# Performance work log

Hardware: AMD Instinct MI355X
Metric: run time of the kernel (lower is better)

Reference implementation:

```python
import jax, jax.numpy as jnp
import numpy as np

BS, SL, D = 4, 2048, 1024
H = 16
HD = D // H  # 64


def setup_inputs() -> dict:
    key = jax.random.key(0)
    ks = jax.random.split(key, 11)
    s = 1.0 / np.sqrt(D)
    inp = {
        "value": jax.random.normal(ks[0], (BS, SL, D), jnp.float32),
        "key_in": jax.random.normal(ks[1], (BS, SL, D), jnp.float32),
        "query": jax.random.normal(ks[2], (BS, SL, D), jnp.float32),
        # nn.Linear weights stored [out, in] (torch convention); orthogonal-ish init approximated by scaled normal
        "Wq": jax.random.normal(ks[3], (D, D), jnp.float32) * s,
        "bq": jax.random.normal(ks[4], (D,), jnp.float32) * 0.01,
        "Wk": jax.random.normal(ks[5], (D, D), jnp.float32) * s,
        "bk": jax.random.normal(ks[6], (D,), jnp.float32) * 0.01,
        "Wv": jax.random.normal(ks[7], (D, D), jnp.float32) * s,
        "bv": jax.random.normal(ks[8], (D,), jnp.float32) * 0.01,
        "Wo": jax.random.normal(ks[9], (D, D), jnp.float32) * s,
        "bo": jax.random.normal(ks[10], (D,), jnp.float32) * 0.01,
    }
    return inp


def reference(value, key_in, query, Wq, bq, Wk, bk, Wv, bv, Wo, bo):
    bs, sl, _ = value.shape
    # projections (torch Linear: x @ W.T + b), then split heads -> [b, h, s, hd]
    def proj(x, W, b):
        return (x @ W.T + b).reshape(bs, -1, H, HD).transpose(0, 2, 1, 3)

    q = proj(query, Wq, bq)
    k = proj(key_in, Wk, bk)
    v = proj(value, Wv, bv)

    scale = 1.0 / jnp.sqrt(jnp.asarray(HD, q.dtype))
    logits = jnp.einsum("bhqd,bhkd->bhqk", q, k) * scale  # [b,h,s,s]
    # amax-subtract + softmax == stable softmax
    attn = jax.nn.softmax(logits, axis=-1)
    out = jnp.einsum("bhqk,bhkd->bhqd", attn, v)
    out = out.transpose(0, 2, 1, 3).reshape(bs, sl, D)  # [b,s,D]
    o = out @ Wo.T + bo
    return o
```

## Files before the change

kernel.cpp:

```cpp
#include <hip/hip_runtime.h>
#include <hip/hip_bf16.h>

typedef __bf16 bf16_t;
typedef __bf16 bf16x8 __attribute__((ext_vector_type(8)));
typedef __bf16 bf16x4 __attribute__((ext_vector_type(4)));
typedef float f32x4 __attribute__((ext_vector_type(4)));
typedef float f32x16 __attribute__((ext_vector_type(16)));

#define BS 4
#define SL 2048
#define DM 1024
#define NH 16
#define HD 64

static __device__ __forceinline__ bf16_t tobf(float x) { return (bf16_t)x; }

#if __has_builtin(__builtin_amdgcn_exp2f)
#define EXP2(x) __builtin_amdgcn_exp2f(x)
#else
#define EXP2(x) exp2f(x)
#endif

#if __has_builtin(__builtin_amdgcn_cvt_pk_bf16_f32)
typedef __bf16 bf16x2_t __attribute__((ext_vector_type(2)));
static __device__ __forceinline__ uint32_t pack_bf16(float a, float b) {
  union { bf16x2_t v; uint32_t u; } c;
  c.v = __builtin_amdgcn_cvt_pk_bf16_f32(a, b);
  return c.u;
}
#else
static __device__ __forceinline__ uint32_t pack_bf16(float a, float b) {
  union { bf16_t e[2]; uint32_t u; } c;
  c.e[0] = tobf(a); c.e[1] = tobf(b);
  return c.u;
}
#endif

static __device__ __forceinline__ void glds16(const void* g, void* l) {
  __builtin_amdgcn_global_load_lds(
      (const __attribute__((address_space(1))) void*)g,
      (__attribute__((address_space(3))) void*)l, 16, 0, 0);
}

#define BAR()    asm volatile("s_barrier" ::: "memory")
#define WAITV0() asm volatile("s_waitcnt vmcnt(0)" ::: "memory")
#define WAITV4() asm volatile("s_waitcnt vmcnt(4)" ::: "memory")
#define WAITLG() asm volatile("s_waitcnt lgkmcnt(0)" ::: "memory")
#define SCHEDB() __builtin_amdgcn_sched_barrier(0)

__global__ void convert_w_kernel(const float* __restrict__ s0, const float* __restrict__ s1,
                                 const float* __restrict__ s2, const float* __restrict__ s3,
                                 bf16_t* __restrict__ d0, bf16_t* __restrict__ d1,
                                 bf16_t* __restrict__ d2, bf16_t* __restrict__ d3)
{
  const float* s; bf16_t* d;
  switch (blockIdx.y) {
    case 0: s = s0; d = d0; break;
    case 1: s = s1; d = d1; break;
    case 2: s = s2; d = d2; break;
    default: s = s3; d = d3; break;
  }
  int i = (blockIdx.x * 256 + threadIdx.x) * 4;
  float4 v = *(const float4*)(s + i);
  bf16x4 o; o[0] = tobf(v.x); o[1] = tobf(v.y); o[2] = tobf(v.z); o[3] = tobf(v.w);
  *(bf16x4*)(d + i) = o;
}

__global__ void convert_a_kernel(const float* __restrict__ q, const float* __restrict__ k,
                                 const float* __restrict__ v, bf16_t* __restrict__ dst)
{
  const float* s = blockIdx.y == 0 ? q : (blockIdx.y == 1 ? k : v);
  bf16_t* d = dst + (size_t)blockIdx.y * ((size_t)BS * SL * DM);
  int i = (blockIdx.x * 256 + threadIdx.x) * 4;
  float4 x = *(const float4*)(s + i);
  bf16x4 o; o[0] = tobf(x.x); o[1] = tobf(x.y); o[2] = tobf(x.z); o[3] = tobf(x.w);
  *(bf16x4*)(d + i) = o;
}

__global__ __launch_bounds__(512, 2) void gemm_qkv_kernel(
    const bf16_t* __restrict__ Aall, const bf16_t* __restrict__ Wcat,
    const float* __restrict__ bq, const float* __restrict__ bk, const float* __restrict__ bvv,
    bf16_t* __restrict__ Qb, bf16_t* __restrict__ Kbo, bf16_t* __restrict__ Vtb)
{
  __shared__ __align__(16) char sMem[131072];

  const int tid  = threadIdx.x;
  const int wave = tid >> 6;
  const int lane = tid & 63;
  const int l15  = lane & 15;
  const int quad = lane >> 4;
  const int wr   = wave >> 2;
  const int wc   = wave & 3;
  const int m0 = blockIdx.x * 256;
  const int nTile = blockIdx.y;
  const int proj = nTile >> 2;
  const int n0 = (nTile & 3) * 256;
  const int nW = nTile * 256;

  const bf16_t* Af = Aall + (size_t)proj * ((size_t)BS * SL * DM);
  const float* bias = proj == 0 ? bq : (proj == 1 ? bk : bvv);

  auto stageA = [&](int u) {
    int tu = u >> 1, kk = u & 1;
    char* dst = sMem + (u & 3) * 16384;
#pragma unroll
    for (int g2 = 0; g2 < 2; g2++) {
      int slot = wave * 2 + g2;
      int f = slot * 64 + lane;
      int row = f >> 2;
      int cg = (f & 3) ^ (row & 3);
      glds16(Af + (size_t)(m0 + row) * DM + tu * 64 + kk * 32 + cg * 8,
             dst + slot * 1024);
    }
  };
  auto stageB = [&](int u) {
    int tu = u >> 1, kk = u & 1;
    char* dst = sMem + 65536 + (u & 3) * 16384;
#pragma unroll
    for (int g2 = 0; g2 < 2; g2++) {
      int slot = wave * 2 + g2;
      int f = slot * 64 + lane;
      int row = f >> 2;
      int cg = (f & 3) ^ (row & 3);
      glds16(Wcat + (size_t)(nW + row) * DM + tu * 64 + kk * 32 + cg * 8,
             dst + slot * 1024);
    }
  };

  f32x4 acc[8][4];
#pragma unroll
  for (int i = 0; i < 8; i++)
#pragma unroll
    for (int j = 0; j < 4; j++) acc[i][j] = f32x4{0.f, 0.f, 0.f, 0.f};

  stageA(0); stageB(0); stageA(1); stageB(1); stageA(2); stageB(2);
  WAITV4(); SCHEDB();
  BAR();

  bf16x8 b[4];
  for (int T = 0; T < 16; ++T) {
#pragma unroll
    for (int p = 0; p < 4; ++p) {
      const int qm = p & 1, kk = p >> 1;
      const int ubuf = (2 * T + kk) & 3;
      const char* ab = sMem + ubuf * 16384;
      const char* bb = sMem + 65536 + ubuf * 16384;

      bf16x8 a[4];
#pragma unroll
      for (int mf = 0; mf < 4; mf++) {
        int row = wr * 128 + qm * 64 + mf * 16 + l15;
        a[mf] = *(const bf16x8*)(ab + row * 64 + ((quad ^ (row & 3)) * 16));
      }
      if (qm == 0) {
#pragma unroll
        for (int nf = 0; nf < 4; nf++) {
          int row = wc * 64 + nf * 16 + l15;
          b[nf] = *(const bf16x8*)(bb + row * 64 + ((quad ^ (row & 3)) * 16));
        }
      }

      if (p == 0)      { int u = 2 * T + 3; if (u < 32) stageA(u); }
      else if (p == 1) { int u = 2 * T + 3; if (u < 32) stageB(u); }
      else if (p == 2) { int u = 2 * T + 4; if (u < 32) stageA(u); }
      else             { int u = 2 * T + 4; if (u < 32) stageB(u); }

      if (p == 3 && T < 15) {
        if (T == 14) { WAITV0(); } else { WAITV4(); }
        SCHEDB();
      }
      BAR();
      WAITLG(); SCHEDB();
      __builtin_amdgcn_s_setprio(1);
#pragma unroll
      for (int mf = 0; mf < 4; mf++)
#pragma unroll
        for (int nf = 0; nf < 4; nf++)
          acc[qm * 4 + mf][nf] = __builtin_amdgcn_mfma_f32_16x16x32_bf16(
              a[mf], b[nf], acc[qm * 4 + mf][nf], 0, 0, 0);
      __builtin_amdgcn_s_setprio(0);
      BAR();
    }
  }

  if (proj < 2) {
    bf16_t* C = proj == 0 ? Qb : Kbo;
#pragma unroll
    for (int nf = 0; nf < 4; nf++) {
      int col = n0 + wc * 64 + nf * 16 + l15;
      float bv = bias[col];
#pragma unroll
      for (int i = 0; i < 8; i++) {
        int rowb = m0 + wr * 128 + (i >> 2) * 64 + (i & 3) * 16 + quad * 4;
#pragma unroll
        for (int r = 0; r < 4; r++)
          C[(size_t)(rowb + r) * DM + col] = tobf(acc[i][nf][r] + bv);
      }
    }
  } else {
#pragma unroll
    for (int nf = 0; nf < 4; nf++) {
      int col = n0 + wc * 64 + nf * 16 + l15;
      float bv = bias[col];
      int head = col >> 6, hd = col & 63;
#pragma unroll
      for (int i = 0; i < 8; i++) {
        int rowb = m0 + wr * 128 + (i >> 2) * 64 + (i & 3) * 16 + quad * 4;
        int bidx = rowb >> 11, s = rowb & (SL - 1);
        bf16x4 o;
#pragma unroll
        for (int r = 0; r < 4; r++) o[r] = tobf(acc[i][nf][r] + bv);
        *(bf16x4*)(Vtb + ((size_t)(bidx * NH + head) * HD + hd) * SL + s) = o;
      }
    }
  }
}

__global__ __launch_bounds__(256, 2) void gemm_out_kernel(
    const bf16_t* __restrict__ A, const bf16_t* __restrict__ Bw,
    const float* __restrict__ bias, float* __restrict__ C)
{
  __shared__ __align__(16) char sMem[32768];

  const int tid  = threadIdx.x;
  const int wave = tid >> 6;
  const int lane = tid & 63;
  const int l15  = lane & 15;
  const int quad = lane >> 4;
  const int m0 = blockIdx.x * 128;
  const int n0 = blockIdx.y * 128;
  const int wm = (wave & 1) * 64;
  const int wn = (wave >> 1) * 64;

  auto stage = [&](int r, int k0) {
    char* base = sMem + r * 16384;
#pragma unroll
    for (int t = 0; t < 2; t++) {
      int slot = wave * 2 + t;
      int f = slot * 64 + lane;
      int row = f >> 2;
      int cg = (f & 3) ^ (row & 3);
      glds16(A  + (size_t)(m0 + row) * DM + k0 + cg * 8, base + slot * 1024);
      glds16(Bw + (size_t)(n0 + row) * DM + k0 + cg * 8, base + 8192 + slot * 1024);
    }
  };

  f32x4 acc[4][4];
#pragma unroll
  for (int i = 0; i < 4; i++)
#pragma unroll
    for (int j = 0; j < 4; j++) acc[i][j] = f32x4{0.f, 0.f, 0.f, 0.f};

  stage(0, 0);
  for (int t = 0; t < 32; ++t) {
    __syncthreads();
    if (t < 31) stage((t + 1) & 1, (t + 1) * 32);

    const bf16_t* sA = (const bf16_t*)(sMem + (t & 1) * 16384);
    const bf16_t* sB = sA + 4096;

    bf16x8 af[4], bfr[4];
#pragma unroll
    for (int i = 0; i < 4; i++) {
      int row = wm + i * 16 + l15;
      af[i] = *(const bf16x8*)(sA + row * 32 + (quad ^ (row & 3)) * 8);
    }
#pragma unroll
    for (int j = 0; j < 4; j++) {
      int row = wn + j * 16 + l15;
      bfr[j] = *(const bf16x8*)(sB + row * 32 + (quad ^ (row & 3)) * 8);
    }

#pragma unroll
    for (int i = 0; i < 4; i++)
#pragma unroll
      for (int j = 0; j < 4; j++)
        acc[i][j] = __builtin_amdgcn_mfma_f32_16x16x32_bf16(af[i], bfr[j], acc[i][j], 0, 0, 0);
  }

#pragma unroll
  for (int j = 0; j < 4; j++) {
    int col = n0 + wn + j * 16 + l15;
    float bv = bias[col];
#pragma unroll
    for (int i = 0; i < 4; i++) {
      int rowb = m0 + wm + i * 16 + quad * 4;
#pragma unroll
      for (int r = 0; r < 4; r++)
        C[(size_t)(rowb + r) * DM + col] = acc[i][j][r] + bv;
    }
  }
}

__global__ __launch_bounds__(256, 4) void attn_kernel(
    const bf16_t* __restrict__ Q, const bf16_t* __restrict__ Kb,
    const bf16_t* __restrict__ Vt, bf16_t* __restrict__ O)
{
  __shared__ __align__(16) char sMem[32768];

  const int tid  = threadIdx.x;
  const int wave = tid >> 6;
  const int lane = tid & 63;
  const int l31  = lane & 31;
  const int h    = lane >> 5;
  const int swl  = l31 & 7;

  const int id  = blockIdx.x;
  const int xcd = id & 7, slot = id >> 3;
  const int bh  = xcd * 8 + (slot >> 4);
  const int qi  = slot & 15;
  const int b = bh >> 4, hh = bh & 15;
  const int q0 = qi * 128 + wave * 32;

  auto stage = [&](int r, int k0) {
    char* base = sMem + r * 16384;
#pragma unroll
    for (int t = 0; t < 2; t++) {
      int slot2 = wave * 2 + t;
      int f = slot2 * 64 + lane;
      int row = f >> 3;
      int cg = (f & 7) ^ ((row + (row >> 3)) & 7);
      glds16(Kb + (size_t)(b * SL + k0 + row) * DM + hh * HD + cg * 8,
             base + slot2 * 1024);
      glds16(Vt + ((size_t)bh * HD + row) * SL + k0 + cg * 8,
             base + 8192 + slot2 * 1024);
    }
  };

  bf16x8 qf[4];
  {
    const bf16_t* qp = Q + (size_t)(b * SL + q0 + l31) * DM + hh * HD + h * 8;
#pragma unroll
    for (int c = 0; c < 4; c++) {
      bf16x8 v = *(const bf16x8*)(qp + c * 16);
#pragma unroll
      for (int j = 0; j < 8; j++) v[j] = tobf((float)v[j] * 0.18033688f);
      qf[c] = v;
    }
  }

  f32x16 o_acc[2];
#pragma unroll
  for (int m = 0; m < 2; m++)
#pragma unroll
    for (int r = 0; r < 16; r++) o_acc[m][r] = 0.f;
  float rs0 = 0.f, rs1 = 0.f;

  stage(0, 0);
  for (int t = 0; t < 32; ++t) {
    __syncthreads();
    if (t < 31) stage((t + 1) & 1, (t + 1) * 64);

    const bf16_t* sK = (const bf16_t*)(sMem + (t & 1) * 16384);
    const bf16_t* sV = sK + 4096;

#pragma unroll
    for (int s = 0; s < 2; s++) {
      int rowK = s * 32 + l31;
      int kkK = (rowK + (rowK >> 3)) & 7;
      bf16x8 kf[4];
#pragma unroll
      for (int c = 0; c < 4; c++)
        kf[c] = *(const bf16x8*)(sK + rowK * 64 + (((c * 2 + h) ^ kkK) * 8));

      f32x16 st;
#pragma unroll
      for (int r = 0; r < 16; r++) st[r] = -17.312340f;
#pragma unroll
      for (int c = 0; c < 4; c++)
        st = __builtin_amdgcn_mfma_f32_32x32x16_bf16(kf[c], qf[c], st, 0, 0, 0);

      uint32_t w[8];
#pragma unroll
      for (int i = 0; i < 8; i++) {
        float p0 = EXP2(st[2 * i]);
        float p1 = EXP2(st[2 * i + 1]);
        rs0 += p0; rs1 += p1;
        w[i] = pack_bf16(p0, p1);
      }
      uint32_t y0 = (uint32_t)__shfl_xor((int)(h ? w[0] : w[2]), 32);
      uint32_t y1 = (uint32_t)__shfl_xor((int)(h ? w[1] : w[3]), 32);
      uint32_t y2 = (uint32_t)__shfl_xor((int)(h ? w[4] : w[6]), 32);
      uint32_t y3 = (uint32_t)__shfl_xor((int)(h ? w[5] : w[7]), 32);
      union { uint32_t u[4]; bf16x8 v; } pf0, pf1;
      pf0.u[0] = h ? y0   : w[0];
      pf0.u[1] = h ? y1   : w[1];
      pf0.u[2] = h ? w[2] : y0;
      pf0.u[3] = h ? w[3] : y1;
      pf1.u[0] = h ? y2   : w[4];
      pf1.u[1] = h ? y3   : w[5];
      pf1.u[2] = h ? w[6] : y2;
      pf1.u[3] = h ? w[7] : y3;

#pragma unroll
      for (int m = 0; m < 2; m++) {
        int rowV = m * 32 + l31;
        int kkV = (rowV + (rowV >> 3)) & 7;
#pragma unroll
        for (int c = 0; c < 2; c++) {
          int chunk = (s * 4 + c * 2 + h) ^ kkV;
          bf16x8 vf = *(const bf16x8*)(sV + rowV * 64 + chunk * 8);
          o_acc[m] = __builtin_amdgcn_mfma_f32_32x32x16_bf16(
              vf, (c ? pf1.v : pf0.v), o_acc[m], 0, 0, 0);
        }
      }
    }
  }

  float rs = rs0 + rs1;
  rs += __shfl_xor(rs, 32);
  float inv = 1.f / rs;
  bf16_t* so = (bf16_t*)sMem + wave * 2048;
#pragma unroll
  for (int m = 0; m < 2; m++) {
#pragma unroll
    for (int r = 0; r < 16; r++) {
      int hd = m * 32 + (r & 3) + 8 * (r >> 2) + 4 * h;
      so[l31 * 64 + (((hd >> 3) ^ swl) * 8) + (hd & 7)] = tobf(o_acc[m][r] * inv);
    }
  }
  asm volatile("s_waitcnt lgkmcnt(0)" ::: "memory");
  {
    int qr = lane >> 1, hf = lane & 1;
    int sw2 = qr & 7;
#pragma unroll
    for (int cc = 0; cc < 4; cc++) {
      int chunk = (hf * 4 + cc) ^ sw2;
      bf16x8 v = *(const bf16x8*)(so + qr * 64 + chunk * 8);
      *(bf16x8*)(O + (size_t)(b * SL + q0 + qr) * DM + hh * HD + hf * 32 + cc * 8) = v;
    }
  }
}

extern "C" void kernel_launch(void* const* d_in, const int* in_sizes, int n_in,
                              void* d_out, int out_size, void* d_ws, size_t ws_size,
                              hipStream_t stream)
{
  const float* value  = (const float*)d_in[0];
  const float* key_in = (const float*)d_in[1];
  const float* query  = (const float*)d_in[2];
  const float* Wq = (const float*)d_in[3];
  const float* bq = (const float*)d_in[4];
  const float* Wk = (const float*)d_in[5];
  const float* bk = (const float*)d_in[6];
  const float* Wv = (const float*)d_in[7];
  const float* bv = (const float*)d_in[8];
  const float* Wo = (const float*)d_in[9];
  const float* bo = (const float*)d_in[10];

  char* ws = (char*)d_ws;
  const size_t sz  = (size_t)BS * SL * DM * sizeof(bf16_t);
  const size_t wsz = (size_t)DM * DM * sizeof(bf16_t);
  bf16_t* Qb   = (bf16_t*)(ws + 0 * sz);
  bf16_t* Kb   = (bf16_t*)(ws + 1 * sz);
  bf16_t* Ob   = (bf16_t*)(ws + 2 * sz);
  bf16_t* Vtb  = (bf16_t*)(ws + 3 * sz);
  bf16_t* Wcat = (bf16_t*)(ws + 4 * sz);
  bf16_t* Wob  = (bf16_t*)(ws + 4 * sz + 3 * wsz);
  bf16_t* Abf  = (bf16_t*)(ws + 4 * sz + 4 * wsz);

  const int M = BS * SL;

  convert_w_kernel<<<dim3(1024, 4), 256, 0, stream>>>(
      Wq, Wk, Wv, Wo, Wcat, Wcat + DM * DM, Wcat + 2 * DM * DM, Wob);

  convert_a_kernel<<<dim3(M * DM / 1024, 3), 256, 0, stream>>>(
      query, key_in, value, Abf);

  gemm_qkv_kernel<<<dim3(M / 256, 12), 512, 0, stream>>>(
      Abf, Wcat, bq, bk, bv, Qb, Kb, Vtb);

  attn_kernel<<<dim3(SL / 128 * BS * NH), 256, 0, stream>>>(Qb, Kb, Vtb, Ob);

  gemm_out_kernel<<<dim3(M / 128, DM / 128), 256, 0, stream>>>(Ob, Wob, bo, (float*)d_out);
}
```

Measured before the change: 359.3 us.

## Retile QKV and output GEMMs, swap lane shuffles for permlane32 swap

The QKV GEMM drops from a 256x256 to a 128x256 tile, with a 4-stage 32-wide K pipeline and a unified A+B staging lambda. This shrinks shared memory and doubles the grid for better CU occupancy. The output GEMM moves from a double-buffered 128x128 tile on 256 threads to the same 512-thread 128x256 pipelined scheme. In attention, the cross-half lane exchange uses v_permlane32_swap instead of ds_bpermute shuffles, and the MFMA blocks get s_setprio boosts. The risk is lower per-block reuse in the QKV GEMM and reliance on the permlane32 swap semantics matching the old select-and-shuffle logic.

```diff
diff --git a/kernel.cpp b/kernel.cpp
--- a/kernel.cpp
+++ b/kernel.cpp
@@ -36,6 +36,10 @@
 }
 #endif
 
+static __device__ __forceinline__ void permswap(uint32_t& a, uint32_t& b) {
+  asm("v_permlane32_swap_b32 %0, %1" : "+v"(a), "+v"(b));
+}
+
 static __device__ __forceinline__ void glds16(const void* g, void* l) {
   __builtin_amdgcn_global_load_lds(
       (const __attribute__((address_space(1))) void*)g,
@@ -44,7 +48,8 @@
 
 #define BAR()    asm volatile("s_barrier" ::: "memory")
 #define WAITV0() asm volatile("s_waitcnt vmcnt(0)" ::: "memory")
-#define WAITV4() asm volatile("s_waitcnt vmcnt(4)" ::: "memory")
+#define WAITV3() asm volatile("s_waitcnt vmcnt(3)" ::: "memory")
+#define WAITV6() asm volatile("s_waitcnt vmcnt(6)" ::: "memory")
 #define WAITLG() asm volatile("s_waitcnt lgkmcnt(0)" ::: "memory")
 #define SCHEDB() __builtin_amdgcn_sched_barrier(0)
 
@@ -82,7 +87,7 @@
     const float* __restrict__ bq, const float* __restrict__ bk, const float* __restrict__ bvv,
     bf16_t* __restrict__ Qb, bf16_t* __restrict__ Kbo, bf16_t* __restrict__ Vtb)
 {
-  __shared__ __align__(16) char sMem[131072];
+  __shared__ __align__(16) char sMem[98304];
 
   const int tid  = threadIdx.x;
   const int wave = tid >> 6;
@@ -91,7 +96,7 @@
   const int quad = lane >> 4;
   const int wr   = wave >> 2;
   const int wc   = wave & 3;
-  const int m0 = blockIdx.x * 256;
+  const int m0 = blockIdx.x * 128;
   const int nTile = blockIdx.y;
   const int proj = nTile >> 2;
   const int n0 = (nTile & 3) * 256;
@@ -100,88 +105,75 @@
   const bf16_t* Af = Aall + (size_t)proj * ((size_t)BS * SL * DM);
   const float* bias = proj == 0 ? bq : (proj == 1 ? bk : bvv);
 
-  auto stageA = [&](int u) {
-    int tu = u >> 1, kk = u & 1;
-    char* dst = sMem + (u & 3) * 16384;
-#pragma unroll
-    for (int g2 = 0; g2 < 2; g2++) {
-      int slot = wave * 2 + g2;
-      int f = slot * 64 + lane;
+  auto stageU = [&](int u) {
+    int k0 = u * 32;
+    {
+      char* dst = sMem + (u & 3) * 8192;
+      int f = wave * 64 + lane;
       int row = f >> 2;
       int cg = (f & 3) ^ (row & 3);
-      glds16(Af + (size_t)(m0 + row) * DM + tu * 64 + kk * 32 + cg * 8,
-             dst + slot * 1024);
+      glds16(Af + (size_t)(m0 + row) * DM + k0 + cg * 8, dst + wave * 1024);
+    }
+    {
+      char* dst = sMem + 32768 + (u & 3) * 16384;
+#pragma unroll
+      for (int g2 = 0; g2 < 2; g2++) {
+        int slot = wave * 2 + g2;
+        int f = slot * 64 + lane;
+        int row = f >> 2;
+        int cg = (f & 3) ^ (row & 3);
+        glds16(Wcat + (size_t)(nW + row) * DM + k0 + cg * 8, dst + slot * 1024);
+      }
     }
   };
-  auto stageB = [&](int u) {
-    int tu = u >> 1, kk = u & 1;
-    char* dst = sMem + 65536 + (u & 3) * 16384;
-#pragma unroll
-    for (int g2 = 0; g2 < 2; g2++) {
-      int slot = wave * 2 + g2;
-      int f = slot * 64 + lane;
-      int row = f >> 2;
-      int cg = (f & 3) ^ (row & 3);
-      glds16(Wcat + (size_t)(nW + row) * DM + tu * 64 + kk * 32 + cg * 8,
-             dst + slot * 1024);
-    }
+
+  f32x4 acc[4][4];
+#pragma unroll
+  for (int i = 0; i < 4; i++)
+#pragma unroll
+    for (int j = 0; j < 4; j++) acc[i][j] = f32x4{0.f, 0.f, 0.f, 0.f};
+
+  stageU(0); stageU(1); stageU(2);
+  WAITV6(); SCHEDB();
+  BAR();
+
+  auto phase = [&](int g, int stageu, int waitn) {
+    const char* ab = sMem + (g & 3) * 8192;
+    const char* bb = sMem + 32768 + (g & 3) * 16384;
+    bf16x8 a[4], b[4];
+#pragma unroll
+    for (int mf = 0; mf < 4; mf++) {
+      int row = wr * 64 + mf * 16 + l15;
+      a[mf] = *(const bf16x8*)(ab + row * 64 + ((quad ^ (row & 3)) * 16));
+    }
+#pragma unroll
+    for (int nf = 0; nf < 4; nf++) {
+      int row = wc * 64 + nf * 16 + l15;
+      b[nf] = *(const bf16x8*)(bb + row * 64 + ((quad ^ (row & 3)) * 16));
+    }
+    if (stageu >= 0) stageU(stageu);
+    if (waitn == 6)      { WAITV6(); SCHEDB(); }
+    else if (waitn == 3) { WAITV3(); SCHEDB(); }
+    else if (waitn == 0) { WAITV0(); SCHEDB(); }
+    BAR();
+    WAITLG(); SCHEDB();
+    __builtin_amdgcn_s_setprio(1);
+#pragma unroll
+    for (int mf = 0; mf < 4; mf++)
+#pragma unroll
+      for (int nf = 0; nf < 4; nf++)
+        acc[mf][nf] = __builtin_amdgcn_mfma_f32_16x16x32_bf16(
+            a[mf], b[nf], acc[mf][nf], 0, 0, 0);
+    __builtin_amdgcn_s_setprio(0);
+    BAR();
   };
 
-  f32x4 acc[8][4];
-#pragma unroll
-  for (int i = 0; i < 8; i++)
-#pragma unroll
-    for (int j = 0; j < 4; j++) acc[i][j] = f32x4{0.f, 0.f, 0.f, 0.f};
-
-  stageA(0); stageB(0); stageA(1); stageB(1); stageA(2); stageB(2);
-  WAITV4(); SCHEDB();
-  BAR();
-
-  bf16x8 b[4];
-  for (int T = 0; T < 16; ++T) {
-#pragma unroll
-    for (int p = 0; p < 4; ++p) {
-      const int qm = p & 1, kk = p >> 1;
-      const int ubuf = (2 * T + kk) & 3;
-      const char* ab = sMem + ubuf * 16384;
-      const char* bb = sMem + 65536 + ubuf * 16384;
-
-      bf16x8 a[4];
-#pragma unroll
-      for (int mf = 0; mf < 4; mf++) {
-        int row = wr * 128 + qm * 64 + mf * 16 + l15;
-        a[mf] = *(const bf16x8*)(ab + row * 64 + ((quad ^ (row & 3)) * 16));
-      }
-      if (qm == 0) {
-#pragma unroll
-        for (int nf = 0; nf < 4; nf++) {
-          int row = wc * 64 + nf * 16 + l15;
-          b[nf] = *(const bf16x8*)(bb + row * 64 + ((quad ^ (row & 3)) * 16));
-        }
-      }
-
-      if (p == 0)      { int u = 2 * T + 3; if (u < 32) stageA(u); }
-      else if (p == 1) { int u = 2 * T + 3; if (u < 32) stageB(u); }
-      else if (p == 2) { int u = 2 * T + 4; if (u < 32) stageA(u); }
-      else             { int u = 2 * T + 4; if (u < 32) stageB(u); }
-
-      if (p == 3 && T < 15) {
-        if (T == 14) { WAITV0(); } else { WAITV4(); }
-        SCHEDB();
-      }
-      BAR();
-      WAITLG(); SCHEDB();
-      __builtin_amdgcn_s_setprio(1);
-#pragma unroll
-      for (int mf = 0; mf < 4; mf++)
-#pragma unroll
-        for (int nf = 0; nf < 4; nf++)
-          acc[qm * 4 + mf][nf] = __builtin_amdgcn_mfma_f32_16x16x32_bf16(
-              a[mf], b[nf], acc[qm * 4 + mf][nf], 0, 0, 0);
-      __builtin_amdgcn_s_setprio(0);
-      BAR();
-    }
-  }
+#pragma unroll 4
+  for (int g = 0; g < 28; ++g) phase(g, g + 3, 6);
+  phase(28, 31, 6);
+  phase(29, -1, 3);
+  phase(30, -1, 0);
+  phase(31, -1, -1);
 
   if (proj < 2) {
     bf16_t* C = proj == 0 ? Qb : Kbo;
@@ -190,11 +182,11 @@
       int col = n0 + wc * 64 + nf * 16 + l15;
       float bv = bias[col];
 #pragma unroll
-      for (int i = 0; i < 8; i++) {
-        int rowb = m0 + wr * 128 + (i >> 2) * 64 + (i & 3) * 16 + quad * 4;
+      for (int mf = 0; mf < 4; mf++) {
+        int rowb = m0 + wr * 64 + mf * 16 + quad * 4;
 #pragma unroll
         for (int r = 0; r < 4; r++)
-          C[(size_t)(rowb + r) * DM + col] = tobf(acc[i][nf][r] + bv);
+          C[(size_t)(rowb + r) * DM + col] = tobf(acc[mf][nf][r] + bv);
       }
     }
   } else {
@@ -204,44 +196,53 @@
       float bv = bias[col];
       int head = col >> 6, hd = col & 63;
 #pragma unroll
-      for (int i = 0; i < 8; i++) {
-        int rowb = m0 + wr * 128 + (i >> 2) * 64 + (i & 3) * 16 + quad * 4;
+      for (int mf = 0; mf < 4; mf++) {
+        int rowb = m0 + wr * 64 + mf * 16 + quad * 4;
         int bidx = rowb >> 11, s = rowb & (SL - 1);
         bf16x4 o;
 #pragma unroll
-        for (int r = 0; r < 4; r++) o[r] = tobf(acc[i][nf][r] + bv);
+        for (int r = 0; r < 4; r++) o[r] = tobf(acc[mf][nf][r] + bv);
         *(bf16x4*)(Vtb + ((size_t)(bidx * NH + head) * HD + hd) * SL + s) = o;
       }
     }
   }
 }
 
-__global__ __launch_bounds__(256, 2) void gemm_out_kernel(
+__global__ __launch_bounds__(512, 2) void gemm_out_kernel(
     const bf16_t* __restrict__ A, const bf16_t* __restrict__ Bw,
     const float* __restrict__ bias, float* __restrict__ C)
 {
-  __shared__ __align__(16) char sMem[32768];
+  __shared__ __align__(16) char sMem[98304];
 
   const int tid  = threadIdx.x;
   const int wave = tid >> 6;
   const int lane = tid & 63;
   const int l15  = lane & 15;
   const int quad = lane >> 4;
+  const int wr   = wave >> 2;
+  const int wc   = wave & 3;
   const int m0 = blockIdx.x * 128;
-  const int n0 = blockIdx.y * 128;
-  const int wm = (wave & 1) * 64;
-  const int wn = (wave >> 1) * 64;
-
-  auto stage = [&](int r, int k0) {
-    char* base = sMem + r * 16384;
-#pragma unroll
-    for (int t = 0; t < 2; t++) {
-      int slot = wave * 2 + t;
-      int f = slot * 64 + lane;
+  const int n0 = blockIdx.y * 256;
+
+  auto stageU = [&](int u) {
+    int k0 = u * 32;
+    {
+      char* dst = sMem + (u & 3) * 8192;
+      int f = wave * 64 + lane;
       int row = f >> 2;
       int cg = (f & 3) ^ (row & 3);
-      glds16(A  + (size_t)(m0 + row) * DM + k0 + cg * 8, base + slot * 1024);
-      glds16(Bw + (size_t)(n0 + row) * DM + k0 + cg * 8, base + 8192 + slot * 1024);
+      glds16(A + (size_t)(m0 + row) * DM + k0 + cg * 8, dst + wave * 1024);
+    }
+    {
+      char* dst = sMem + 32768 + (u & 3) * 16384;
+#pragma unroll
+      for (int g2 = 0; g2 < 2; g2++) {
+        int slot = wave * 2 + g2;
+        int f = slot * 64 + lane;
+        int row = f >> 2;
+        int cg = (f & 3) ^ (row & 3);
+        glds16(Bw + (size_t)(n0 + row) * DM + k0 + cg * 8, dst + slot * 1024);
+      }
     }
   };
 
@@ -251,43 +252,58 @@
 #pragma unroll
     for (int j = 0; j < 4; j++) acc[i][j] = f32x4{0.f, 0.f, 0.f, 0.f};
 
-  stage(0, 0);
-  for (int t = 0; t < 32; ++t) {
-    __syncthreads();
-    if (t < 31) stage((t + 1) & 1, (t + 1) * 32);
-
-    const bf16_t* sA = (const bf16_t*)(sMem + (t & 1) * 16384);
-    const bf16_t* sB = sA + 4096;
-
-    bf16x8 af[4], bfr[4];
-#pragma unroll
-    for (int i = 0; i < 4; i++) {
-      int row = wm + i * 16 + l15;
-      af[i] = *(const bf16x8*)(sA + row * 32 + (quad ^ (row & 3)) * 8);
-    }
-#pragma unroll
-    for (int j = 0; j < 4; j++) {
-      int row = wn + j * 16 + l15;
-      bfr[j] = *(const bf16x8*)(sB + row * 32 + (quad ^ (row & 3)) * 8);
-    }
-
-#pragma unroll
-    for (int i = 0; i < 4; i++)
-#pragma unroll
-      for (int j = 0; j < 4; j++)
-        acc[i][j] = __builtin_amdgcn_mfma_f32_16x16x32_bf16(af[i], bfr[j], acc[i][j], 0, 0, 0);
-  }
-
-#pragma unroll
-  for (int j = 0; j < 4; j++) {
-    int col = n0 + wn + j * 16 + l15;
+  stageU(0); stageU(1); stageU(2);
+  WAITV6(); SCHEDB();
+  BAR();
+
+  auto phase = [&](int g, int stageu, int waitn) {
+    const char* ab = sMem + (g & 3) * 8192;
+    const char* bb = sMem + 32768 + (g & 3) * 16384;
+    bf16x8 a[4], b[4];
+#pragma unroll
+    for (int mf = 0; mf < 4; mf++) {
+      int row = wr * 64 + mf * 16 + l15;
+      a[mf] = *(const bf16x8*)(ab + row * 64 + ((quad ^ (row & 3)) * 16));
+    }
+#pragma unroll
+    for (int nf = 0; nf < 4; nf++) {
+      int row = wc * 64 + nf * 16 + l15;
+      b[nf] = *(const bf16x8*)(bb + row * 64 + ((quad ^ (row & 3)) * 16));
+    }
+    if (stageu >= 0) stageU(stageu);
+    if (waitn == 6)      { WAITV6(); SCHEDB(); }
+    else if (waitn == 3) { WAITV3(); SCHEDB(); }
+    else if (waitn == 0) { WAITV0(); SCHEDB(); }
+    BAR();
+    WAITLG(); SCHEDB();
+    __builtin_amdgcn_s_setprio(1);
+#pragma unroll
+    for (int mf = 0; mf < 4; mf++)
+#pragma unroll
+      for (int nf = 0; nf < 4; nf++)
+        acc[mf][nf] = __builtin_amdgcn_mfma_f32_16x16x32_bf16(
+            a[mf], b[nf], acc[mf][nf], 0, 0, 0);
+    __builtin_amdgcn_s_setprio(0);
+    BAR();
+  };
+
+#pragma unroll 4
+  for (int g = 0; g < 28; ++g) phase(g, g + 3, 6);
+  phase(28, 31, 6);
+  phase(29, -1, 3);
+  phase(30, -1, 0);
+  phase(31, -1, -1);
+
+#pragma unroll
+  for (int nf = 0; nf < 4; nf++) {
+    int col = n0 + wc * 64 + nf * 16 + l15;
     float bv = bias[col];
 #pragma unroll
-    for (int i = 0; i < 4; i++) {
-      int rowb = m0 + wm + i * 16 + quad * 4;
+    for (int mf = 0; mf < 4; mf++) {
+      int rowb = m0 + wr * 64 + mf * 16 + quad * 4;
 #pragma unroll
       for (int r = 0; r < 4; r++)
-        C[(size_t)(rowb + r) * DM + col] = acc[i][j][r] + bv;
+        C[(size_t)(rowb + r) * DM + col] = acc[mf][nf][r] + bv;
     }
   }
 }
@@ -366,9 +382,11 @@
       f32x16 st;
 #pragma unroll
       for (int r = 0; r < 16; r++) st[r] = -17.312340f;
+      __builtin_amdgcn_s_setprio(1);
 #pragma unroll
       for (int c = 0; c < 4; c++)
         st = __builtin_amdgcn_mfma_f32_32x32x16_bf16(kf[c], qf[c], st, 0, 0, 0);
+      __builtin_amdgcn_s_setprio(0);
 
       uint32_t w[8];
 #pragma unroll
@@ -378,20 +396,17 @@
         rs0 += p0; rs1 += p1;
         w[i] = pack_bf16(p0, p1);
       }
-      uint32_t y0 = (uint32_t)__shfl_xor((int)(h ? w[0] : w[2]), 32);
-      uint32_t y1 = (uint32_t)__shfl_xor((int)(h ? w[1] : w[3]), 32);
-      uint32_t y2 = (uint32_t)__shfl_xor((int)(h ? w[4] : w[6]), 32);
-      uint32_t y3 = (uint32_t)__shfl_xor((int)(h ? w[5] : w[7]), 32);
       union { uint32_t u[4]; bf16x8 v; } pf0, pf1;
-      pf0.u[0] = h ? y0   : w[0];
-      pf0.u[1] = h ? y1   : w[1];
-      pf0.u[2] = h ? w[2] : y0;
-      pf0.u[3] = h ? w[3] : y1;
-      pf1.u[0] = h ? y2   : w[4];
-      pf1.u[1] = h ? y3   : w[5];
-      pf1.u[2] = h ? w[6] : y2;
-      pf1.u[3] = h ? w[7] : y3;
-
+      {
+        uint32_t a0 = w[0], b0 = w[2]; permswap(a0, b0);
+        uint32_t a1 = w[1], b1 = w[3]; permswap(a1, b1);
+        uint32_t a2 = w[4], b2 = w[6]; permswap(a2, b2);
+        uint32_t a3 = w[5], b3 = w[7]; permswap(a3, b3);
+        pf0.u[0] = a0; pf0.u[1] = a1; pf0.u[2] = b0; pf0.u[3] = b1;
+        pf1.u[0] = a2; pf1.u[1] = a3; pf1.u[2] = b2; pf1.u[3] = b3;
+      }
+
+      __builtin_amdgcn_s_setprio(1);
 #pragma unroll
       for (int m = 0; m < 2; m++) {
         int rowV = m * 32 + l31;
@@ -404,6 +419,7 @@
               vf, (c ? pf1.v : pf0.v), o_acc[m], 0, 0, 0);
         }
       }
+      __builtin_amdgcn_s_setprio(0);
     }
   }
 
@@ -467,10 +483,10 @@
   convert_a_kernel<<<dim3(M * DM / 1024, 3), 256, 0, stream>>>(
       query, key_in, value, Abf);
 
-  gemm_qkv_kernel<<<dim3(M / 256, 12), 512, 0, stream>>>(
+  gemm_qkv_kernel<<<dim3(M / 128, 12), 512, 0, stream>>>(
       Abf, Wcat, bq, bk, bv, Qb, Kb, Vtb);
 
   attn_kernel<<<dim3(SL / 128 * BS * NH), 256, 0, stream>>>(Qb, Kb, Vtb, Ob);
 
-  gemm_out_kernel<<<dim3(M / 128, DM / 128), 256, 0, stream>>>(Ob, Wob, bo, (float*)d_out);
-}
+  gemm_out_kernel<<<dim3(M / 128, DM / 256), 512, 0, stream>>>(Ob, Wob, bo, (float*)d_out);
+}
```

Result: faster. 332.3 us (-7.5%).
